# Kernel optimization log

Hardware: AMD Instinct MI355X
Metric: run time of the kernel (lower is better)

Reference implementation:

```python
import jax, jax.numpy as jnp
import numpy as np

N, E = 8000, 128000
IN_DIM = OUT_DIM = REL_DIM = 64
NUM_RELS, NUM_BASES = 200, 50
R2 = 2 * NUM_RELS


def setup_inputs() -> dict:
    key = jax.random.key(0)
    ks = jax.random.split(key, 10)
    feat = jax.random.normal(ks[0], (N, IN_DIM), jnp.float32)
    rel_emb = jax.random.normal(ks[1], (R2, REL_DIM), jnp.float32)
    weight = jax.random.normal(ks[2], (NUM_BASES, IN_DIM, OUT_DIM), jnp.float32) * 0.05
    w_comp = jax.random.normal(ks[3], (R2, NUM_BASES), jnp.float32) * 0.1
    self_loop_weight = jax.random.normal(ks[4], (IN_DIM, OUT_DIM), jnp.float32) * 0.05
    W_R_w = jax.random.normal(ks[5], (REL_DIM, REL_DIM), jnp.float32) * 0.05
    W_R_b = jnp.zeros((REL_DIM,), jnp.float32)
    src = jax.random.randint(ks[6], (E,), 0, N, dtype=jnp.int32)
    dst = jax.random.randint(ks[7], (E,), 0, N, dtype=jnp.int32)
    etype = jax.random.randint(ks[8], (E,), 0, R2, dtype=jnp.int32)
    return dict(feat=feat, rel_emb=rel_emb, weight=weight, w_comp=w_comp,
                self_loop_weight=self_loop_weight, W_R_w=W_R_w, W_R_b=W_R_b,
                src=src, dst=dst, etype=etype)


def reference(feat, rel_emb, weight, w_comp, self_loop_weight, W_R_w, W_R_b,
              src, dst, etype):
    # rel_weight = (w_comp @ weight.view(B, in*out)).view(R2, in, out)
    rel_weight = jnp.einsum('rb,bio->rio', w_comp, weight)          # [R2, in, out]
    # msg_func: per-edge relation weight gather + bmm (gather-mm pattern)
    w_e = rel_weight[etype]                                          # [E, in, out]
    msg = jnp.einsum('ei,eio->eo', feat[src], w_e)                   # [E, out]
    # aggregator: alpha = 1/in_deg(dst) per edge -> weighted sum == mean over mailbox
    ones = jnp.ones((msg.shape[0],), msg.dtype)
    in_deg = jax.ops.segment_sum(ones, dst, num_segments=N)          # [N]
    nei_sum = jax.ops.segment_sum(msg, dst, num_segments=N)          # [N, out]
    nei_msg = nei_sum / jnp.maximum(in_deg, 1.0)[:, None]
    # curr_emb = dst_feat @ self_loop_weight (same for every edge into a node)
    curr_emb = feat @ self_loop_weight                               # [N, out]
    h = curr_emb + nei_msg                                           # no bias / no activation
    # is_input_layer=True: repr = cat([feat, h])
    repr_ = jnp.concatenate([feat, h], axis=1)                       # [N, in+out]
    # edge_update: W_R linear on relation embeddings (act is None)
    rel_emb_new = rel_emb @ W_R_w.T + W_R_b                          # [R2, rel_dim]
    return repr_, rel_emb_new
```

## Files before the change

kernel.cpp:

```cpp
#include <hip/hip_runtime.h>

#define N_NODES 8000
#define E_EDGES 128000
#define NUM_BASES 50
#define R2 400
#define CPR 4
#define RT 16

static __device__ __forceinline__ float bcast(float v, int lane) {
    return __uint_as_float(__builtin_amdgcn_readlane(__float_as_uint(v), lane));
}

__global__ __launch_bounds__(256) void k_pre(const float* __restrict__ w_comp,
                                             const float* __restrict__ weight,
                                             float* __restrict__ relW,
                                             const int* __restrict__ dst,
                                             const int* __restrict__ etype,
                                             int* __restrict__ cnt16,
                                             float* __restrict__ in_deg) {
    const int blk = blockIdx.x;
    const int t = threadIdx.x;
    if (blk < 100) {
        const int rt = blk >> 2;
        const int pb = blk & 3;
        const int r0 = rt * RT;
        const int p = pb * 256 + t;
        const float4* w4 = (const float4*)weight;
        float4 acc[RT];
#pragma unroll
        for (int rr = 0; rr < RT; ++rr) acc[rr] = make_float4(0.f, 0.f, 0.f, 0.f);
        for (int b = 0; b < NUM_BASES; ++b) {
            const float4 w = w4[b * 1024 + p];
#pragma unroll
            for (int rr = 0; rr < RT; ++rr) {
                const float c = w_comp[(r0 + rr) * NUM_BASES + b];
                acc[rr].x = fmaf(c, w.x, acc[rr].x);
                acc[rr].y = fmaf(c, w.y, acc[rr].y);
                acc[rr].z = fmaf(c, w.z, acc[rr].z);
                acc[rr].w = fmaf(c, w.w, acc[rr].w);
            }
        }
        float4* out4 = (float4*)relW;
#pragma unroll
        for (int rr = 0; rr < RT; ++rr) out4[(r0 + rr) * 1024 + p] = acc[rr];
    } else {
        const int e = (blk - 100) * 256 + t;
        if (e >= E_EDGES) return;
        atomicAdd(&cnt16[etype[e] * 16], 1);
        atomicAdd(&in_deg[dst[e]], 1.0f);
    }
}

__global__ __launch_bounds__(512) void k_scan(const int* __restrict__ cnt16,
                                              int* __restrict__ off) {
    __shared__ int s[512];
    const int t = threadIdx.x;
    s[t] = (t < R2) ? cnt16[t * 16] : 0;
    __syncthreads();
    for (int d = 1; d < 512; d <<= 1) {
        const int v = (t >= d) ? s[t - d] : 0;
        __syncthreads();
        s[t] += v;
        __syncthreads();
    }
    if (t == 0) off[0] = 0;
    if (t < R2) off[t + 1] = s[t];
}

__global__ __launch_bounds__(256) void k_scatter(const int* __restrict__ src,
                                                 const int* __restrict__ dst,
                                                 const int* __restrict__ etype,
                                                 const int* __restrict__ off,
                                                 int* __restrict__ cursor16,
                                                 int* __restrict__ ssrc,
                                                 int* __restrict__ sdst) {
    const int e = blockIdx.x * 256 + threadIdx.x;
    if (e >= E_EDGES) return;
    const int r = etype[e];
    const int pos = off[r] + atomicAdd(&cursor16[r * 16], 1);
    ssrc[pos] = src[e];
    sdst[pos] = dst[e];
}

__global__ __launch_bounds__(256) void k_edge2(const float* __restrict__ feat,
                                               const float* __restrict__ relW,
                                               const int* __restrict__ ssrc,
                                               const int* __restrict__ sdst,
                                               const int* __restrict__ off,
                                               float* __restrict__ nei_sum) {
    const int xcd = blockIdx.x & 7;
    const int j = blockIdx.x >> 3;
    const int r = xcd * 50 + (j >> 2);
    const int chunk = j & 3;
    const int lane = threadIdx.x & 63;
    const int wv = threadIdx.x >> 6;
    const int beg = off[r];
    const int cnt = off[r + 1] - beg;
    const int cbeg = beg + (cnt * chunk) / CPR;
    const int cend = beg + (cnt * (chunk + 1)) / CPR;

    const float* __restrict__ W = relW + r * 4096;
    float w[64];
#pragma unroll
    for (int i = 0; i < 64; ++i) w[i] = W[i * 64 + lane];

    for (int idx = cbeg + wv; idx < cend; idx += 4) {
        const int s = __builtin_amdgcn_readfirstlane(ssrc[idx]);
        const int d = __builtin_amdgcn_readfirstlane(sdst[idx]);
        const float* __restrict__ frow = feat + s * 64;
        float a0 = 0.f, a1 = 0.f, a2 = 0.f, a3 = 0.f;
#pragma unroll
        for (int i = 0; i < 64; i += 4) {
            a0 = fmaf(frow[i    ], w[i    ], a0);
            a1 = fmaf(frow[i + 1], w[i + 1], a1);
            a2 = fmaf(frow[i + 2], w[i + 2], a2);
            a3 = fmaf(frow[i + 3], w[i + 3], a3);
        }
        atomicAdd(&nei_sum[d * 64 + lane], (a0 + a1) + (a2 + a3));
    }
}

__global__ __launch_bounds__(256) void k_post(const float* __restrict__ feat,
                                              const float* __restrict__ slw,
                                              const float* __restrict__ nei_sum,
                                              const float* __restrict__ in_deg,
                                              const float* __restrict__ rel_emb,
                                              const float* __restrict__ Wr,
                                              const float* __restrict__ br,
                                              float* __restrict__ out) {
    const int blk = blockIdx.x;
    const int t = threadIdx.x;
    const int lane = t & 63;
    const int wid = t >> 6;
    if (blk < 2000) {
        __shared__ float s_w[4096];
#pragma unroll
        for (int k = 0; k < 16; ++k) s_w[k * 256 + t] = slw[k * 256 + t];
        __syncthreads();
        const int n = blk * 4 + wid;
        const int nu = __builtin_amdgcn_readfirstlane(n);
        const float* __restrict__ frow = feat + nu * 64;
        const float fa = frow[lane];
        float acc = 0.f;
#pragma unroll
        for (int i = 0; i < 64; ++i) {
            acc = fmaf(frow[i], s_w[i * 64 + lane], acc);
        }
        const float deg = in_deg[nu];
        const float nm = nei_sum[nu * 64 + lane] / fmaxf(deg, 1.0f);
        out[nu * 128 + lane] = fa;
        out[nu * 128 + 64 + lane] = acc + nm;
    } else {
        __shared__ float s_wt[4096];
#pragma unroll
        for (int k = 0; k < 16; ++k) {
            const int idx = k * 256 + t;
            s_wt[(idx & 63) * 64 + (idx >> 6)] = Wr[idx];
        }
        __syncthreads();
        const int r = (blk - 2000) * 4 + wid;
        const float re = rel_emb[r * 64 + lane];
        float acc = br[lane];
#pragma unroll
        for (int k = 0; k < 64; ++k) {
            acc = fmaf(bcast(re, k), s_wt[k * 64 + lane], acc);
        }
        out[N_NODES * 128 + r * 64 + lane] = acc;
    }
}

extern "C" void kernel_launch(void* const* d_in, const int* in_sizes, int n_in,
                              void* d_out, int out_size, void* d_ws, size_t ws_size,
                              hipStream_t stream) {
    const float* feat    = (const float*)d_in[0];
    const float* rel_emb = (const float*)d_in[1];
    const float* weight  = (const float*)d_in[2];
    const float* w_comp  = (const float*)d_in[3];
    const float* slw     = (const float*)d_in[4];
    const float* Wr      = (const float*)d_in[5];
    const float* br      = (const float*)d_in[6];
    const int*   src     = (const int*)d_in[7];
    const int*   dst     = (const int*)d_in[8];
    const int*   etype   = (const int*)d_in[9];
    float* out = (float*)d_out;

    char* ws = (char*)d_ws;
    float* relW     = (float*)(ws);
    float* nei_sum  = (float*)(ws + 6553600);
    float* in_deg   = (float*)(ws + 8601600);
    int*   cnt16    = (int*)  (ws + 8633600);
    int*   cursor16 = (int*)  (ws + 8659200);
    int*   off      = (int*)  (ws + 8684800);
    int*   ssrc     = (int*)  (ws + 8686464);
    int*   sdst     = (int*)  (ws + 9198464);

    hipMemsetAsync(nei_sum, 0, 2048000 + 32000 + 25600 + 25600, stream);

    k_pre<<<600, 256, 0, stream>>>(w_comp, weight, relW, dst, etype, cnt16, in_deg);
    k_scan<<<1, 512, 0, stream>>>(cnt16, off);
    k_scatter<<<E_EDGES / 256, 256, 0, stream>>>(src, dst, etype, off, cursor16,
                                                 ssrc, sdst);
    k_edge2<<<R2 * CPR, 256, 0, stream>>>(feat, relW, ssrc, sdst, off, nei_sum);
    k_post<<<2100, 256, 0, stream>>>(feat, slw, nei_sum, in_deg, rel_emb, Wr, br,
                                     out);
}
```

Before: 103.3 us.

## Replace atomic scatter with dst-sorted bf16 message gather and bf16 relation weights

Relation weights are now stored as bf16, and per-edge messages are written as bf16 into a relation-sorted buffer instead of atomically added into nei_sum. A dst-sorted permutation (dst counts, a second scan, and extra scatter work) lets the post kernel sum each node's messages without atomics. The edge loop processes two edges per wave iteration for more ILP, and the post kernel handles 16 nodes per block. The aim is to remove float atomics and cut weight traffic, at the cost of extra scan/scatter work, a 16MB message round-trip, and reduced precision. A fallback path keeps atomics when the workspace is too small.

```diff
diff --git a/kernel.cpp b/kernel.cpp
--- a/kernel.cpp
+++ b/kernel.cpp
@@ -7,17 +7,25 @@
 #define CPR 4
 #define RT 16
 
+static __device__ __forceinline__ float bf2f(unsigned short u) {
+    return __uint_as_float(((unsigned int)u) << 16);
+}
+static __device__ __forceinline__ unsigned short f2bf(float f) {
+    unsigned int u = __float_as_uint(f);
+    u += 0x7fffu + ((u >> 16) & 1u);
+    return (unsigned short)(u >> 16);
+}
 static __device__ __forceinline__ float bcast(float v, int lane) {
     return __uint_as_float(__builtin_amdgcn_readlane(__float_as_uint(v), lane));
 }
 
 __global__ __launch_bounds__(256) void k_pre(const float* __restrict__ w_comp,
                                              const float* __restrict__ weight,
-                                             float* __restrict__ relW,
+                                             unsigned short* __restrict__ relWh,
                                              const int* __restrict__ dst,
                                              const int* __restrict__ etype,
                                              int* __restrict__ cnt16,
-                                             float* __restrict__ in_deg) {
+                                             int* __restrict__ dcnt) {
     const int blk = blockIdx.x;
     const int t = threadIdx.x;
     if (blk < 100) {
@@ -40,54 +48,91 @@
                 acc[rr].w = fmaf(c, w.w, acc[rr].w);
             }
         }
-        float4* out4 = (float4*)relW;
-#pragma unroll
-        for (int rr = 0; rr < RT; ++rr) out4[(r0 + rr) * 1024 + p] = acc[rr];
+        ushort4* outh = (ushort4*)relWh;
+#pragma unroll
+        for (int rr = 0; rr < RT; ++rr) {
+            ushort4 v;
+            v.x = f2bf(acc[rr].x); v.y = f2bf(acc[rr].y);
+            v.z = f2bf(acc[rr].z); v.w = f2bf(acc[rr].w);
+            outh[(r0 + rr) * 1024 + p] = v;
+        }
     } else {
         const int e = (blk - 100) * 256 + t;
         if (e >= E_EDGES) return;
         atomicAdd(&cnt16[etype[e] * 16], 1);
-        atomicAdd(&in_deg[dst[e]], 1.0f);
-    }
-}
-
-__global__ __launch_bounds__(512) void k_scan(const int* __restrict__ cnt16,
-                                              int* __restrict__ off) {
-    __shared__ int s[512];
+        atomicAdd(&dcnt[dst[e]], 1);
+    }
+}
+
+__global__ __launch_bounds__(1024) void k_scan(const int* __restrict__ cnt16,
+                                               const int* __restrict__ dcnt,
+                                               int* __restrict__ off,
+                                               int* __restrict__ doff) {
+    __shared__ int s[1024];
     const int t = threadIdx.x;
-    s[t] = (t < R2) ? cnt16[t * 16] : 0;
-    __syncthreads();
-    for (int d = 1; d < 512; d <<= 1) {
-        const int v = (t >= d) ? s[t - d] : 0;
-        __syncthreads();
-        s[t] += v;
-        __syncthreads();
-    }
-    if (t == 0) off[0] = 0;
-    if (t < R2) off[t + 1] = s[t];
+    if (blockIdx.x == 0) {
+        s[t] = (t < R2) ? cnt16[t * 16] : 0;
+        __syncthreads();
+        for (int d = 1; d < 1024; d <<= 1) {
+            const int v = (t >= d) ? s[t - d] : 0;
+            __syncthreads();
+            s[t] += v;
+            __syncthreads();
+        }
+        if (t == 0) off[0] = 0;
+        if (t < R2) off[t + 1] = s[t];
+    } else {
+        const int base = t * 8;
+        int loc[8];
+        int run = 0;
+#pragma unroll
+        for (int q = 0; q < 8; ++q) {
+            const int v = (base + q < N_NODES) ? dcnt[base + q] : 0;
+            loc[q] = run;
+            run += v;
+        }
+        s[t] = run;
+        __syncthreads();
+        for (int d = 1; d < 1024; d <<= 1) {
+            const int v = (t >= d) ? s[t - d] : 0;
+            __syncthreads();
+            s[t] += v;
+            __syncthreads();
+        }
+        const int ex = s[t] - run;
+#pragma unroll
+        for (int q = 0; q < 8; ++q)
+            if (base + q < N_NODES) doff[base + q] = ex + loc[q];
+        if (t == 1023) doff[N_NODES] = s[1023];
+    }
 }
 
 __global__ __launch_bounds__(256) void k_scatter(const int* __restrict__ src,
                                                  const int* __restrict__ dst,
                                                  const int* __restrict__ etype,
                                                  const int* __restrict__ off,
+                                                 const int* __restrict__ doff,
                                                  int* __restrict__ cursor16,
+                                                 int* __restrict__ dcursor,
                                                  int* __restrict__ ssrc,
-                                                 int* __restrict__ sdst) {
+                                                 int* __restrict__ sdst,
+                                                 int* __restrict__ dperm) {
     const int e = blockIdx.x * 256 + threadIdx.x;
     if (e >= E_EDGES) return;
     const int r = etype[e];
-    const int pos = off[r] + atomicAdd(&cursor16[r * 16], 1);
-    ssrc[pos] = src[e];
-    sdst[pos] = dst[e];
-}
-
-__global__ __launch_bounds__(256) void k_edge2(const float* __restrict__ feat,
-                                               const float* __restrict__ relW,
-                                               const int* __restrict__ ssrc,
-                                               const int* __restrict__ sdst,
-                                               const int* __restrict__ off,
-                                               float* __restrict__ nei_sum) {
+    const int rpos = off[r] + atomicAdd(&cursor16[r * 16], 1);
+    ssrc[rpos] = src[e];
+    sdst[rpos] = dst[e];
+    const int d = dst[e];
+    const int dpos = doff[d] + atomicAdd(&dcursor[d], 1);
+    dperm[dpos] = rpos;
+}
+
+__global__ __launch_bounds__(256) void k_edge(const float* __restrict__ feat,
+                                              const unsigned short* __restrict__ relWh,
+                                              const int* __restrict__ ssrc,
+                                              const int* __restrict__ off,
+                                              unsigned short* __restrict__ msg) {
     const int xcd = blockIdx.x & 7;
     const int j = blockIdx.x >> 3;
     const int r = xcd * 50 + (j >> 2);
@@ -99,10 +144,66 @@
     const int cbeg = beg + (cnt * chunk) / CPR;
     const int cend = beg + (cnt * (chunk + 1)) / CPR;
 
-    const float* __restrict__ W = relW + r * 4096;
+    const unsigned short* __restrict__ Wh = relWh + r * 4096;
     float w[64];
 #pragma unroll
-    for (int i = 0; i < 64; ++i) w[i] = W[i * 64 + lane];
+    for (int i = 0; i < 64; ++i) w[i] = bf2f(Wh[i * 64 + lane]);
+
+    int idx = cbeg + wv;
+    for (; idx + 4 < cend; idx += 8) {
+        const int iB = idx + 4;
+        const int sA = __builtin_amdgcn_readfirstlane(ssrc[idx]);
+        const int sB = __builtin_amdgcn_readfirstlane(ssrc[iB]);
+        const float* __restrict__ fA = feat + sA * 64;
+        const float* __restrict__ fB = feat + sB * 64;
+        float a0 = 0.f, a1 = 0.f, a2 = 0.f, a3 = 0.f;
+        float b0 = 0.f, b1 = 0.f, b2 = 0.f, b3 = 0.f;
+#pragma unroll
+        for (int i = 0; i < 64; i += 4) {
+            a0 = fmaf(fA[i    ], w[i    ], a0);  b0 = fmaf(fB[i    ], w[i    ], b0);
+            a1 = fmaf(fA[i + 1], w[i + 1], a1);  b1 = fmaf(fB[i + 1], w[i + 1], b1);
+            a2 = fmaf(fA[i + 2], w[i + 2], a2);  b2 = fmaf(fB[i + 2], w[i + 2], b2);
+            a3 = fmaf(fA[i + 3], w[i + 3], a3);  b3 = fmaf(fB[i + 3], w[i + 3], b3);
+        }
+        msg[idx * 64 + lane] = f2bf((a0 + a1) + (a2 + a3));
+        msg[iB * 64 + lane] = f2bf((b0 + b1) + (b2 + b3));
+    }
+    for (; idx < cend; idx += 4) {
+        const int s = __builtin_amdgcn_readfirstlane(ssrc[idx]);
+        const float* __restrict__ frow = feat + s * 64;
+        float a0 = 0.f, a1 = 0.f, a2 = 0.f, a3 = 0.f;
+#pragma unroll
+        for (int i = 0; i < 64; i += 4) {
+            a0 = fmaf(frow[i    ], w[i    ], a0);
+            a1 = fmaf(frow[i + 1], w[i + 1], a1);
+            a2 = fmaf(frow[i + 2], w[i + 2], a2);
+            a3 = fmaf(frow[i + 3], w[i + 3], a3);
+        }
+        msg[idx * 64 + lane] = f2bf((a0 + a1) + (a2 + a3));
+    }
+}
+
+__global__ __launch_bounds__(256) void k_edge_at(const float* __restrict__ feat,
+                                                 const unsigned short* __restrict__ relWh,
+                                                 const int* __restrict__ ssrc,
+                                                 const int* __restrict__ sdst,
+                                                 const int* __restrict__ off,
+                                                 float* __restrict__ nei_sum) {
+    const int xcd = blockIdx.x & 7;
+    const int j = blockIdx.x >> 3;
+    const int r = xcd * 50 + (j >> 2);
+    const int chunk = j & 3;
+    const int lane = threadIdx.x & 63;
+    const int wv = threadIdx.x >> 6;
+    const int beg = off[r];
+    const int cnt = off[r + 1] - beg;
+    const int cbeg = beg + (cnt * chunk) / CPR;
+    const int cend = beg + (cnt * (chunk + 1)) / CPR;
+
+    const unsigned short* __restrict__ Wh = relWh + r * 4096;
+    float w[64];
+#pragma unroll
+    for (int i = 0; i < 64; ++i) w[i] = bf2f(Wh[i * 64 + lane]);
 
     for (int idx = cbeg + wv; idx < cend; idx += 4) {
         const int s = __builtin_amdgcn_readfirstlane(ssrc[idx]);
@@ -122,49 +223,105 @@
 
 __global__ __launch_bounds__(256) void k_post(const float* __restrict__ feat,
                                               const float* __restrict__ slw,
-                                              const float* __restrict__ nei_sum,
-                                              const float* __restrict__ in_deg,
+                                              const int* __restrict__ doff,
+                                              const int* __restrict__ dperm,
+                                              const unsigned short* __restrict__ msg,
                                               const float* __restrict__ rel_emb,
                                               const float* __restrict__ Wr,
                                               const float* __restrict__ br,
                                               float* __restrict__ out) {
+    __shared__ float s_w[4096];
     const int blk = blockIdx.x;
     const int t = threadIdx.x;
     const int lane = t & 63;
-    const int wid = t >> 6;
-    if (blk < 2000) {
-        __shared__ float s_w[4096];
+    const int wv = t >> 6;
+    if (blk < 500) {
 #pragma unroll
         for (int k = 0; k < 16; ++k) s_w[k * 256 + t] = slw[k * 256 + t];
         __syncthreads();
-        const int n = blk * 4 + wid;
-        const int nu = __builtin_amdgcn_readfirstlane(n);
-        const float* __restrict__ frow = feat + nu * 64;
-        const float fa = frow[lane];
-        float acc = 0.f;
-#pragma unroll
-        for (int i = 0; i < 64; ++i) {
-            acc = fmaf(frow[i], s_w[i * 64 + lane], acc);
-        }
-        const float deg = in_deg[nu];
-        const float nm = nei_sum[nu * 64 + lane] / fmaxf(deg, 1.0f);
-        out[nu * 128 + lane] = fa;
-        out[nu * 128 + 64 + lane] = acc + nm;
-    } else {
-        __shared__ float s_wt[4096];
+#pragma unroll
+        for (int q = 0; q < 4; ++q) {
+            const int n = blk * 16 + wv * 4 + q;
+            const int b0 = doff[n];
+            const int b1 = doff[n + 1];
+            const float* __restrict__ frow = feat + n * 64;
+            const float fa = frow[lane];
+            float acc = 0.f;
+#pragma unroll
+            for (int i = 0; i < 64; ++i)
+                acc = fmaf(frow[i], s_w[i * 64 + lane], acc);
+            float sm = 0.f;
+            int jj = b0;
+            for (; jj + 1 < b1; jj += 2) {
+                const int r0 = dperm[jj];
+                const int r1 = dperm[jj + 1];
+                sm += bf2f(msg[r0 * 64 + lane]) + bf2f(msg[r1 * 64 + lane]);
+            }
+            if (jj < b1) sm += bf2f(msg[dperm[jj] * 64 + lane]);
+            const float inv = 1.0f / fmaxf((float)(b1 - b0), 1.0f);
+            out[n * 128 + lane] = fa;
+            out[n * 128 + 64 + lane] = fmaf(sm, inv, acc);
+        }
+    } else {
 #pragma unroll
         for (int k = 0; k < 16; ++k) {
             const int idx = k * 256 + t;
-            s_wt[(idx & 63) * 64 + (idx >> 6)] = Wr[idx];
-        }
-        __syncthreads();
-        const int r = (blk - 2000) * 4 + wid;
+            s_w[(idx & 63) * 64 + (idx >> 6)] = Wr[idx];
+        }
+        __syncthreads();
+        const int r = (blk - 500) * 4 + wv;
         const float re = rel_emb[r * 64 + lane];
         float acc = br[lane];
 #pragma unroll
-        for (int k = 0; k < 64; ++k) {
-            acc = fmaf(bcast(re, k), s_wt[k * 64 + lane], acc);
-        }
+        for (int k = 0; k < 64; ++k)
+            acc = fmaf(bcast(re, k), s_w[k * 64 + lane], acc);
+        out[N_NODES * 128 + r * 64 + lane] = acc;
+    }
+}
+
+__global__ __launch_bounds__(256) void k_post_at(const float* __restrict__ feat,
+                                                 const float* __restrict__ slw,
+                                                 const float* __restrict__ nei_sum,
+                                                 const int* __restrict__ dcnt,
+                                                 const float* __restrict__ rel_emb,
+                                                 const float* __restrict__ Wr,
+                                                 const float* __restrict__ br,
+                                                 float* __restrict__ out) {
+    __shared__ float s_w[4096];
+    const int blk = blockIdx.x;
+    const int t = threadIdx.x;
+    const int lane = t & 63;
+    const int wv = t >> 6;
+    if (blk < 500) {
+#pragma unroll
+        for (int k = 0; k < 16; ++k) s_w[k * 256 + t] = slw[k * 256 + t];
+        __syncthreads();
+#pragma unroll
+        for (int q = 0; q < 4; ++q) {
+            const int n = blk * 16 + wv * 4 + q;
+            const float* __restrict__ frow = feat + n * 64;
+            const float fa = frow[lane];
+            float acc = 0.f;
+#pragma unroll
+            for (int i = 0; i < 64; ++i)
+                acc = fmaf(frow[i], s_w[i * 64 + lane], acc);
+            const float inv = 1.0f / fmaxf((float)dcnt[n], 1.0f);
+            out[n * 128 + lane] = fa;
+            out[n * 128 + 64 + lane] = fmaf(nei_sum[n * 64 + lane], inv, acc);
+        }
+    } else {
+#pragma unroll
+        for (int k = 0; k < 16; ++k) {
+            const int idx = k * 256 + t;
+            s_w[(idx & 63) * 64 + (idx >> 6)] = Wr[idx];
+        }
+        __syncthreads();
+        const int r = (blk - 500) * 4 + wv;
+        const float re = rel_emb[r * 64 + lane];
+        float acc = br[lane];
+#pragma unroll
+        for (int k = 0; k < 64; ++k)
+            acc = fmaf(bcast(re, k), s_w[k * 64 + lane], acc);
         out[N_NODES * 128 + r * 64 + lane] = acc;
     }
 }
@@ -183,24 +340,51 @@
     const int*   dst     = (const int*)d_in[8];
     const int*   etype   = (const int*)d_in[9];
     float* out = (float*)d_out;
-
     char* ws = (char*)d_ws;
-    float* relW     = (float*)(ws);
-    float* nei_sum  = (float*)(ws + 6553600);
-    float* in_deg   = (float*)(ws + 8601600);
-    int*   cnt16    = (int*)  (ws + 8633600);
-    int*   cursor16 = (int*)  (ws + 8659200);
-    int*   off      = (int*)  (ws + 8684800);
-    int*   ssrc     = (int*)  (ws + 8686464);
-    int*   sdst     = (int*)  (ws + 9198464);
-
-    hipMemsetAsync(nei_sum, 0, 2048000 + 32000 + 25600 + 25600, stream);
-
-    k_pre<<<600, 256, 0, stream>>>(w_comp, weight, relW, dst, etype, cnt16, in_deg);
-    k_scan<<<1, 512, 0, stream>>>(cnt16, off);
-    k_scatter<<<E_EDGES / 256, 256, 0, stream>>>(src, dst, etype, off, cursor16,
-                                                 ssrc, sdst);
-    k_edge2<<<R2 * CPR, 256, 0, stream>>>(feat, relW, ssrc, sdst, off, nei_sum);
-    k_post<<<2100, 256, 0, stream>>>(feat, slw, nei_sum, in_deg, rel_emb, Wr, br,
-                                     out);
-}
+
+    if (ws_size >= 21345728) {
+        unsigned short* relWh = (unsigned short*)(ws);
+        unsigned short* msg   = (unsigned short*)(ws + 3276800);
+        int* ssrc     = (int*)(ws + 19660800);
+        int* sdst     = (int*)(ws + 20172800);
+        int* dperm    = (int*)(ws + 20684800);
+        int* off      = (int*)(ws + 21196800);
+        int* doff     = (int*)(ws + 21198464);
+        int* cnt16    = (int*)(ws + 21230528);
+        int* cursor16 = (int*)(ws + 21256128);
+        int* dcnt     = (int*)(ws + 21281728);
+        int* dcursor  = (int*)(ws + 21313728);
+
+        hipMemsetAsync(cnt16, 0, 115200, stream);
+        k_pre<<<600, 256, 0, stream>>>(w_comp, weight, relWh, dst, etype,
+                                       cnt16, dcnt);
+        k_scan<<<2, 1024, 0, stream>>>(cnt16, dcnt, off, doff);
+        k_scatter<<<500, 256, 0, stream>>>(src, dst, etype, off, doff,
+                                           cursor16, dcursor, ssrc, sdst, dperm);
+        k_edge<<<R2 * CPR, 256, 0, stream>>>(feat, relWh, ssrc, off, msg);
+        k_post<<<600, 256, 0, stream>>>(feat, slw, doff, dperm, msg,
+                                        rel_emb, Wr, br, out);
+    } else {
+        unsigned short* relWh = (unsigned short*)(ws);
+        int* ssrc     = (int*)(ws + 3276800);
+        int* sdst     = (int*)(ws + 3788800);
+        int* dperm    = (int*)(ws + 4300800);
+        int* off      = (int*)(ws + 4812800);
+        int* doff     = (int*)(ws + 4814464);
+        float* nei    = (float*)(ws + 4846528);
+        int* cnt16    = (int*)(ws + 6894528);
+        int* cursor16 = (int*)(ws + 6920128);
+        int* dcnt     = (int*)(ws + 6945728);
+        int* dcursor  = (int*)(ws + 6977728);
+
+        hipMemsetAsync(nei, 0, 2163200, stream);
+        k_pre<<<600, 256, 0, stream>>>(w_comp, weight, relWh, dst, etype,
+                                       cnt16, dcnt);
+        k_scan<<<2, 1024, 0, stream>>>(cnt16, dcnt, off, doff);
+        k_scatter<<<500, 256, 0, stream>>>(src, dst, etype, off, doff,
+                                           cursor16, dcursor, ssrc, sdst, dperm);
+        k_edge_at<<<R2 * CPR, 256, 0, stream>>>(feat, relWh, ssrc, sdst, off, nei);
+        k_post_at<<<600, 256, 0, stream>>>(feat, slw, nei, dcnt,
+                                           rel_emb, Wr, br, out);
+    }
+}
```

Measured after the change: 124.7 us. 20.7% more time.
